# Kernel tuning notes

Measured on AMD Instinct MI355X. Metric: run time of the kernel, lower is better.

The kernel has to match this reference:

```python
import jax, jax.numpy as jnp
import numpy as np

_EPS = 1e-5
_NH, _DH = 4, 64  # heads, dim_head


def _ln(x, g, b):
    m = x.mean(-1, keepdims=True)
    v = ((x - m) ** 2).mean(-1, keepdims=True)
    return (x - m) / jnp.sqrt(v + _EPS) * g + b


def _leaky(x):
    return jnp.where(x > 0, x, 0.01 * x)


def _bn_eval(x, g, b):
    # eval-mode BatchNorm with running_mean=0, running_var=1
    return x * (g / np.sqrt(1.0 + _EPS)) + b


def setup_inputs() -> dict:
    key = jax.random.key(0)
    ks = jax.random.split(key, 20)
    B, L, S, D, T, H = 4096, 8, 877, 256, 137, 128
    f = jnp.float32

    def rn(k, shape, s=0.02):
        return jax.random.normal(k, shape, dtype=f) * s

    inp = {}
    inp['source'] = jax.random.normal(ks[0], (B, S), dtype=f)
    inp['source_neighbor'] = jax.random.normal(ks[1], (B, L, S), dtype=f)
    inp['cell_inf'] = jax.random.uniform(ks[2], (B, L + 1, 13), dtype=f)
    # encoder_rna: 877 -> 512 -> 256, Linear+BN(eval)+LeakyReLU
    inp['enc_w1'] = rn(ks[3], (S, 512)); inp['enc_b1'] = jnp.zeros((512,), f)
    inp['enc_bn1_g'] = jnp.ones((512,), f); inp['enc_bn1_b'] = jnp.zeros((512,), f)
    inp['enc_w2'] = rn(ks[4], (512, D)); inp['enc_b2'] = jnp.zeros((D,), f)
    inp['enc_bn2_g'] = jnp.ones((D,), f); inp['enc_bn2_b'] = jnp.zeros((D,), f)
    # projection_rna: Linear(256,256) + LayerNorm + ReLU
    inp['proj_w'] = rn(ks[5], (D, D)); inp['proj_b'] = jnp.zeros((D,), f)
    inp['proj_ln_g'] = jnp.ones((D,), f); inp['proj_ln_b'] = jnp.zeros((D,), f)
    # 1-layer pre-norm transformer (4 heads, dim_head 64, ff_mult 2)
    inp['attn_ln_g'] = jnp.ones((D,), f); inp['attn_ln_b'] = jnp.zeros((D,), f)
    inp['wq'] = rn(ks[6], (D, D)); inp['wk'] = rn(ks[7], (D, D)); inp['wv'] = rn(ks[8], (D, D))
    inp['wo'] = rn(ks[9], (D, D)); inp['wo_b'] = jnp.zeros((D,), f)
    inp['ff_ln_g'] = jnp.ones((D,), f); inp['ff_ln_b'] = jnp.zeros((D,), f)
    inp['ff_w1'] = rn(ks[10], (D, 2 * D)); inp['ff_b1'] = jnp.zeros((2 * D,), f)
    inp['ff_w2'] = rn(ks[11], (2 * D, D)); inp['ff_b2'] = jnp.zeros((D,), f)
    # learned tokens
    inp['token_center'] = rn(ks[12], (1, 1, D))
    inp['token_neigh_1'] = rn(ks[13], (1, 1, D))
    inp['token_neigh_2'] = rn(ks[14], (1, 1, D))
    inp['cell_tokens'] = rn(ks[15], (1, 1, 13, D))
    # 137 independent predict heads, batched: Linear(256,128)+BN+LeakyReLU+Linear(128,1,no bias)
    inp['pred_w1'] = rn(ks[16], (T, D, H)); inp['pred_b1'] = jnp.zeros((T, H), f)
    inp['pred_bn_g'] = jnp.ones((T, H), f); inp['pred_bn_b'] = jnp.zeros((T, H), f)
    inp['pred_w2'] = rn(ks[17], (T, H))
    return inp


def _forward(source, source_neighbor, cell_inf, enc_w1, enc_b1, enc_bn1_g, enc_bn1_b,
             enc_w2, enc_b2, enc_bn2_g, enc_bn2_b, proj_w, proj_b, proj_ln_g, proj_ln_b,
             attn_ln_g, attn_ln_b, wq, wk, wv, wo, wo_b, ff_ln_g, ff_ln_b,
             ff_w1, ff_b1, ff_w2, ff_b2, token_center, token_neigh_1, token_neigh_2,
             cell_tokens, pred_w1, pred_b1, pred_bn_g, pred_bn_b, pred_w2):
    B = source.shape[0]
    x = jnp.concatenate([source[:, None, :], source_neighbor], axis=1)  # [B,N,877]
    N = x.shape[1]
    l = N - 1
    half = l // 2
    valid = jnp.abs(x).sum(-1) > 0                      # [B,N] bool
    vm = valid.astype(x.dtype)[..., None]               # [B,N,1]
    D = token_center.shape[-1]
    # role tokens: center / first-half neigh / second-half neigh, masked
    role = jnp.concatenate([
        token_center,
        jnp.broadcast_to(token_neigh_1, (1, half, D)),
        jnp.broadcast_to(token_neigh_2, (1, l - half, D)),
    ], axis=1) * vm                                      # [B,N,D]
    # class tokens: weighted sum over 13 cell-type tokens, masked
    class_tok = (cell_tokens * cell_inf[..., None]).sum(-2) * vm  # [B,N,D]
    # encoder_rna (dropouts are eval identity)
    h = _leaky(_bn_eval(x @ enc_w1 + enc_b1, enc_bn1_g, enc_bn1_b))
    h = _leaky(_bn_eval(h @ enc_w2 + enc_b2, enc_bn2_g, enc_bn2_b))  # [B,N,D]
    fo = h + role + class_tok
    fo = jax.nn.relu(_ln(fo @ proj_w + proj_b, proj_ln_g, proj_ln_b))
    # local graph transformer encoder (depth=1, pre-norm, masked attention)
    hn = _ln(fo, attn_ln_g, attn_ln_b)
    q = (hn @ wq).reshape(B, N, _NH, _DH)
    k = (hn @ wk).reshape(B, N, _NH, _DH)
    v = (hn @ wv).reshape(B, N, _NH, _DH)
    scores = jnp.einsum('bihd,bjhd->bhij', q, k) * (_DH ** -0.5)
    scores = jnp.where(valid[:, None, None, :], scores, -1e9)
    attn = jax.nn.softmax(scores, axis=-1)
    o = jnp.einsum('bhij,bjhd->bihd', attn, v).reshape(B, N, _NH * _DH)
    fo = fo + o @ wo + wo_b
    hn2 = _ln(fo, ff_ln_g, ff_ln_b)
    fo = fo + jax.nn.gelu(hn2 @ ff_w1 + ff_b1) @ ff_w2 + ff_b2
    feat = fo[:, 0, :]                                   # [B,D] center token
    # 137 predict heads as one batched GEMM + fused BN/LeakyReLU
    ph = jnp.einsum('bd,tdh->bth', feat, pred_w1) + pred_b1   # [B,137,128]
    ph = _leaky(_bn_eval(ph, pred_bn_g, pred_bn_b))
    out = jnp.einsum('bth,th->bt', ph, pred_w2)               # [B,137]
    return out


def reference(source, source_neighbor, cell_inf, enc_w1, enc_b1, enc_bn1_g, enc_bn1_b,
              enc_w2, enc_b2, enc_bn2_g, enc_bn2_b, proj_w, proj_b, proj_ln_g, proj_ln_b,
              attn_ln_g, attn_ln_b, wq, wk, wv, wo, wo_b, ff_ln_g, ff_ln_b,
              ff_w1, ff_b1, ff_w2, ff_b2, token_center, token_neigh_1, token_neigh_2,
              cell_tokens, pred_w1, pred_b1, pred_bn_g, pred_bn_b, pred_w2):
    return _forward(source, source_neighbor, cell_inf, enc_w1, enc_b1, enc_bn1_g, enc_bn1_b,
                    enc_w2, enc_b2, enc_bn2_g, enc_bn2_b, proj_w, proj_b, proj_ln_g, proj_ln_b,
                    attn_ln_g, attn_ln_b, wq, wk, wv, wo, wo_b, ff_ln_g, ff_ln_b,
                    ff_w1, ff_b1, ff_w2, ff_b2, token_center, token_neigh_1, token_neigh_2,
                    cell_tokens, pred_w1, pred_b1, pred_bn_g, pred_bn_b, pred_w2)
```

## Files before the change

kernel.cpp:

```cpp
#include <hip/hip_runtime.h>
#include <hip/hip_bf16.h>
#include <math.h>

typedef __hip_bfloat16 bf16;
typedef __attribute__((ext_vector_type(8))) short short8;
typedef __attribute__((ext_vector_type(4))) float f32x4;

#define BB 4096
#define LL 8
#define NN 9
#define SS 877
#define DD 256
#define D2 512
#define TT 137
#define HH 128
#define MM (BB*NN)
#define KP1 896

__device__ __forceinline__ float lrelu(float x){ return x > 0.f ? x : 0.01f*x; }
__device__ __forceinline__ float gelu_tanh(float x){
    float x3 = x*x*x;
    float t = tanhf(0.7978845608028654f*(x + 0.044715f*x3));
    return 0.5f*x*(1.f + t);
}
__device__ __forceinline__ short f2b(float x){
    union { bf16 h; short s; } u; u.h = __float2bfloat16(x); return u.s;
}
__device__ __forceinline__ float b2f(bf16 v){ return __bfloat162float(v); }

struct SwzD { const float* src; unsigned short* dst; int K; int N; int NB; long long base; };
struct SwzTab { SwzD d[10]; long long total; };

__global__ __launch_bounds__(256) void k_swzall(SwzTab tab){
    for (long long f0 = (long long)blockIdx.x*256 + threadIdx.x; f0 < tab.total;
         f0 += (long long)gridDim.x*256){
        int di = 0;
        #pragma unroll
        for (int q = 1; q < 10; q++) if (f0 >= tab.d[q].base) di = q;
        const SwzD dd = tab.d[di];
        long long f = f0 - dd.base;
        int j = (int)(f & 7); int lane = (int)((f>>3)&63); int h = (int)((f>>9)&7);
        long long u = f>>12;
        int nb = (int)(u % dd.NB), kb = (int)(u / dd.NB);
        int k = kb*32 + ((lane>>4)<<3) + j;
        int n = nb*128 + h*16 + (lane&15);
        float v = (k < dd.K) ? dd.src[(size_t)k*dd.N + n] : 0.f;
        dd.dst[f] = (unsigned short)f2b(v);
    }
}

__global__ __launch_bounds__(256) void k_prep(const float* __restrict__ src,
                                              const float* __restrict__ srcn,
                                              float* __restrict__ vm,
                                              unsigned short* __restrict__ xbf){
    int m = blockIdx.x; int b = m / NN, n = m % NN;
    const float* row = (n == 0) ? src + (size_t)b*SS
                                : srcn + ((size_t)b*LL + (n-1))*SS;
    unsigned short* orow = xbf + (size_t)m*KP1;
    float s = 0.f;
    for (int i = threadIdx.x; i < KP1; i += 256){
        float v = (i < SS) ? row[i] : 0.f;
        s += fabsf(v);
        orow[i] = (unsigned short)f2b(v);
    }
    #pragma unroll
    for (int o = 32; o > 0; o >>= 1) s += __shfl_xor(s, o);
    __shared__ float part[4];
    if ((threadIdx.x & 63) == 0) part[threadIdx.x>>6] = s;
    __syncthreads();
    if (threadIdx.x == 0)
        vm[m] = ((part[0]+part[1]+part[2]+part[3]) > 0.f) ? 1.f : 0.f;
}

#define EPI_NONE 0
#define EPI_BN_LEAKY 1
#define EPI_RES 2
#define EPI_GELU 3

__global__ __launch_bounds__(256) void k_mgemm(
    const unsigned short* __restrict__ A, int lda,
    const unsigned short* __restrict__ Wsw, int NB, int nKb,
    const float* __restrict__ bias, const float* __restrict__ bng,
    const float* __restrict__ bnb, const float* __restrict__ res,
    int res_stride, int mode,
    float* __restrict__ out, bf16* __restrict__ outbf, int ldo)
{
    __shared__ short8 As[512];
    int row0 = blockIdx.x*128;
    int nb = blockIdx.y;
    int tid = threadIdx.x;
    int wv = tid>>6, lane = tid&63;
    int wr = wv>>1, wc = wv&1;
    int quad = lane>>4, l15 = lane&15;

    f32x4 zz = {0.f,0.f,0.f,0.f};
    f32x4 acc[4][4];
    #pragma unroll
    for (int i=0;i<4;i++){ acc[i][0]=zz; acc[i][1]=zz; acc[i][2]=zz; acc[i][3]=zz; }

    int m0 = tid>>2, k8 = tid&3;
    int m1 = m0 + 64;
    int dst0 = (m0>>4)*64 + (m0&15) + (k8<<4);
    int dst1 = (m1>>4)*64 + (m1&15) + (k8<<4);
    const short8* W8 = (const short8*)Wsw;

    for (int kb = 0; kb < nKb; kb++){
        int k0 = kb*32;
        uint4 v0 = *(const uint4*)(A + (size_t)(row0+m0)*lda + k0 + k8*8);
        uint4 v1 = *(const uint4*)(A + (size_t)(row0+m1)*lda + k0 + k8*8);
        short8 bfr[4];
        #pragma unroll
        for (int h = 0; h < 4; h++)
            bfr[h] = W8[((size_t)(kb*NB + nb)*8 + wc*4 + h)*64 + lane];
        __syncthreads();
        ((uint4*)As)[dst0] = v0;
        ((uint4*)As)[dst1] = v1;
        __syncthreads();
        #pragma unroll
        for (int i = 0; i < 4; i++){
            short8 af = As[(wr*4+i)*64 + lane];
            #pragma unroll
            for (int h = 0; h < 4; h++)
                acc[i][h] = __builtin_amdgcn_mfma_f32_16x16x32_bf16(af, bfr[h], acc[i][h], 0,0,0);
        }
    }

    const float inv = rsqrtf(1.f + 1e-5f);
    #pragma unroll
    for (int i = 0; i < 4; i++){
        int rbase = row0 + wr*64 + i*16 + quad*4;
        #pragma unroll
        for (int h = 0; h < 4; h++){
            int c = nb*128 + wc*64 + h*16 + l15;
            float bi = bias ? bias[c] : 0.f;
            #pragma unroll
            for (int reg = 0; reg < 4; reg++){
                int r = rbase + reg;
                float y = acc[i][h][reg] + bi;
                if (mode == EPI_BN_LEAKY)      y = lrelu(y*(bng[c]*inv) + bnb[c]);
                else if (mode == EPI_RES)      y += res[(size_t)r*res_stride + c];
                else if (mode == EPI_GELU)     y = gelu_tanh(y);
                if (out)   out[(size_t)r*ldo + c] = y;
                if (outbf) outbf[(size_t)r*ldo + c] = __float2bfloat16(y);
            }
        }
    }
}

__global__ __launch_bounds__(256) void k_pred_mfma(
    const unsigned short* __restrict__ feat,
    const unsigned short* __restrict__ Wsw,
    const float* __restrict__ b1, const float* __restrict__ bg,
    const float* __restrict__ bb, const float* __restrict__ w2,
    float* __restrict__ outp)
{
    __shared__ short8 As[512];
    int row0 = blockIdx.x*128;
    int t = blockIdx.y;
    int tid = threadIdx.x;
    int wv = tid>>6, lane = tid&63;
    int quad = lane>>4, l15 = lane&15;

    const float inv = rsqrtf(1.f + 1e-5f);
    float b1v[8], bgv[8], bbv[8], w2v[8];
    #pragma unroll
    for (int h = 0; h < 8; h++){
        int hc = t*HH + h*16 + l15;
        b1v[h] = b1[hc]; bgv[h] = bg[hc]*inv; bbv[h] = bb[hc]; w2v[h] = w2[hc];
    }

    f32x4 zz = {0.f,0.f,0.f,0.f};
    f32x4 acc[2][8];
    #pragma unroll
    for (int i=0;i<2;i++)
        #pragma unroll
        for (int h=0;h<8;h++) acc[i][h] = zz;

    int m0 = tid>>2, k8 = tid&3;
    int m1 = m0 + 64;
    int dst0 = (m0>>4)*64 + (m0&15) + (k8<<4);
    int dst1 = (m1>>4)*64 + (m1&15) + (k8<<4);
    const short8* W8 = (const short8*)Wsw;

    for (int kb = 0; kb < 8; kb++){
        int k0 = kb*32;
        uint4 v0 = *(const uint4*)(feat + (size_t)(row0+m0)*DD + k0 + k8*8);
        uint4 v1 = *(const uint4*)(feat + (size_t)(row0+m1)*DD + k0 + k8*8);
        short8 bfr[8];
        #pragma unroll
        for (int h = 0; h < 8; h++)
            bfr[h] = W8[((size_t)(t*8 + kb)*8 + h)*64 + lane];
        __syncthreads();
        ((uint4*)As)[dst0] = v0;
        ((uint4*)As)[dst1] = v1;
        __syncthreads();
        #pragma unroll
        for (int i = 0; i < 2; i++){
            short8 af = As[(wv*2+i)*64 + lane];
            #pragma unroll
            for (int h = 0; h < 8; h++)
                acc[i][h] = __builtin_amdgcn_mfma_f32_16x16x32_bf16(af, bfr[h], acc[i][h], 0,0,0);
        }
    }

    #pragma unroll
    for (int i = 0; i < 2; i++){
        #pragma unroll
        for (int reg = 0; reg < 4; reg++){
            float p = 0.f;
            #pragma unroll
            for (int h = 0; h < 8; h++){
                float y = (acc[i][h][reg] + b1v[h])*bgv[h] + bbv[h];
                p += lrelu(y) * w2v[h];
            }
            p += __shfl_xor(p, 1);
            p += __shfl_xor(p, 2);
            p += __shfl_xor(p, 4);
            p += __shfl_xor(p, 8);
            if (l15 == 0){
                int r = row0 + wv*32 + i*16 + quad*4 + reg;
                outp[(size_t)r*TT + t] = p;
            }
        }
    }
}

__global__ __launch_bounds__(256) void k_rolecls(const float* __restrict__ tokc,
                                                 const float* __restrict__ tokn1,
                                                 const float* __restrict__ tokn2,
                                                 const float* __restrict__ cell_tokens,
                                                 const float* __restrict__ cell_inf,
                                                 const float* __restrict__ vm,
                                                 float* __restrict__ fo,
                                                 bf16* __restrict__ fobf){
    int m = blockIdx.x, d = threadIdx.x;
    int n = m % NN;
    float v = vm[m];
    const float* role = (n == 0) ? tokc : (n <= 4 ? tokn1 : tokn2);
    float cl = 0.f;
    #pragma unroll
    for (int c = 0; c < 13; c++)
        cl += cell_inf[(size_t)m*13 + c] * cell_tokens[c*DD + d];
    float y = fo[(size_t)m*DD + d] + (role[d] + cl) * v;
    fo[(size_t)m*DD + d] = y;
    fobf[(size_t)m*DD + d] = __float2bfloat16(y);
}

__device__ __forceinline__ float blksum(float v, float* part){
    #pragma unroll
    for (int o = 32; o > 0; o >>= 1) v += __shfl_xor(v, o);
    __syncthreads();
    if ((threadIdx.x & 63) == 0) part[threadIdx.x>>6] = v;
    __syncthreads();
    return part[0]+part[1]+part[2]+part[3];
}

__global__ __launch_bounds__(256) void k_lnchain(const float* __restrict__ in,
                                                 const float* __restrict__ g1, const float* __restrict__ b1,
                                                 const float* __restrict__ g2, const float* __restrict__ b2,
                                                 float* __restrict__ fo1, bf16* __restrict__ hn){
    __shared__ float part[4];
    int m = blockIdx.x, d = threadIdx.x;
    float x = in[(size_t)m*DD + d];
    float mu = blksum(x, part) * (1.f/256.f);
    float dx = x - mu;
    float var = blksum(dx*dx, part) * (1.f/256.f);
    float y = dx * rsqrtf(var + 1e-5f) * g1[d] + b1[d];
    y = fmaxf(y, 0.f);
    fo1[(size_t)m*DD + d] = y;
    float mu2 = blksum(y, part) * (1.f/256.f);
    float dy = y - mu2;
    float var2 = blksum(dy*dy, part) * (1.f/256.f);
    hn[(size_t)m*DD + d] = __float2bfloat16(dy * rsqrtf(var2 + 1e-5f) * g2[d] + b2[d]);
}

__global__ __launch_bounds__(256) void k_ln(const float* __restrict__ in,
                                            const float* __restrict__ g, const float* __restrict__ b,
                                            bf16* __restrict__ out){
    __shared__ float part[4];
    int m = blockIdx.x, d = threadIdx.x;
    float x = in[(size_t)m*DD + d];
    float mu = blksum(x, part) * (1.f/256.f);
    float dx = x - mu;
    float var = blksum(dx*dx, part) * (1.f/256.f);
    out[(size_t)m*DD + d] = __float2bfloat16(dx * rsqrtf(var + 1e-5f) * g[d] + b[d]);
}

__global__ __launch_bounds__(256) void k_attn(const bf16* __restrict__ q,
                                              const bf16* __restrict__ k,
                                              const bf16* __restrict__ v,
                                              const float* __restrict__ vm,
                                              bf16* __restrict__ o){
    int b = blockIdx.x, t = threadIdx.x;
    __shared__ float ks[NN][DD];
    __shared__ float vs[NN][DD];
    __shared__ float qs[DD];
    __shared__ float sc[4][NN];
    __shared__ float val[NN];
    qs[t] = b2f(q[(size_t)b*DD + t]);
    for (int j = 0; j < NN; j++){
        ks[j][t] = b2f(k[((size_t)b*NN + j)*DD + t]);
        vs[j][t] = b2f(v[((size_t)b*NN + j)*DD + t]);
    }
    if (t < NN) val[t] = vm[b*NN + t];
    __syncthreads();
    if (t < 4*NN){
        int h = t / NN, j = t % NN;
        float s = 0.f;
        for (int d = 0; d < 64; d++) s += qs[h*64+d] * ks[j][h*64+d];
        s *= 0.125f;
        if (!(val[j] > 0.f)) s = -1e9f;
        sc[h][j] = s;
    }
    __syncthreads();
    if (t < 4){
        float mx = -1e30f;
        for (int j = 0; j < NN; j++) mx = fmaxf(mx, sc[t][j]);
        float den = 0.f;
        for (int j = 0; j < NN; j++){ float e = expf(sc[t][j]-mx); sc[t][j] = e; den += e; }
        float iv = 1.f/den;
        for (int j = 0; j < NN; j++) sc[t][j] *= iv;
    }
    __syncthreads();
    int h = t >> 6;
    float acc = 0.f;
    for (int j = 0; j < NN; j++) acc += sc[h][j] * vs[j][t];
    o[(size_t)b*DD + t] = __float2bfloat16(acc);
}

extern "C" void kernel_launch(void* const* d_in, const int* in_sizes, int n_in,
                              void* d_out, int out_size, void* d_ws, size_t ws_size,
                              hipStream_t stream) {
    const float* src      = (const float*)d_in[0];
    const float* srcn     = (const float*)d_in[1];
    const float* cell_inf = (const float*)d_in[2];
    const float* enc_w1   = (const float*)d_in[3];
    const float* enc_b1   = (const float*)d_in[4];
    const float* bn1g     = (const float*)d_in[5];
    const float* bn1b     = (const float*)d_in[6];
    const float* enc_w2   = (const float*)d_in[7];
    const float* enc_b2   = (const float*)d_in[8];
    const float* bn2g     = (const float*)d_in[9];
    const float* bn2b     = (const float*)d_in[10];
    const float* proj_w   = (const float*)d_in[11];
    const float* proj_b   = (const float*)d_in[12];
    const float* pln_g    = (const float*)d_in[13];
    const float* pln_b    = (const float*)d_in[14];
    const float* aln_g    = (const float*)d_in[15];
    const float* aln_b    = (const float*)d_in[16];
    const float* wq       = (const float*)d_in[17];
    const float* wk       = (const float*)d_in[18];
    const float* wv       = (const float*)d_in[19];
    const float* wo       = (const float*)d_in[20];
    const float* wo_b     = (const float*)d_in[21];
    const float* fln_g    = (const float*)d_in[22];
    const float* fln_b    = (const float*)d_in[23];
    const float* ff_w1    = (const float*)d_in[24];
    const float* ff_b1    = (const float*)d_in[25];
    const float* ff_w2    = (const float*)d_in[26];
    const float* ff_b2    = (const float*)d_in[27];
    const float* tokc     = (const float*)d_in[28];
    const float* tokn1    = (const float*)d_in[29];
    const float* tokn2    = (const float*)d_in[30];
    const float* cell_tok = (const float*)d_in[31];
    const float* pw1      = (const float*)d_in[32];
    const float* pb1      = (const float*)d_in[33];
    const float* pbg      = (const float*)d_in[34];
    const float* pbb      = (const float*)d_in[35];
    const float* pw2      = (const float*)d_in[36];
    float* out            = (float*)d_out;

    char* base = (char*)d_ws;
    size_t off = 0;
    auto alloc = [&](size_t bytes)->char*{
        char* p = base + off;
        off += (bytes + 255) & ~(size_t)255;
        return p;
    };
    bf16* sw_enc1 = (bf16*)alloc((size_t)KP1*D2*2);
    bf16* sw_enc2 = (bf16*)alloc((size_t)D2*DD*2);
    bf16* sw_proj = (bf16*)alloc((size_t)DD*DD*2);
    bf16* sw_wq   = (bf16*)alloc((size_t)DD*DD*2);
    bf16* sw_wk   = (bf16*)alloc((size_t)DD*DD*2);
    bf16* sw_wv   = (bf16*)alloc((size_t)DD*DD*2);
    bf16* sw_wo   = (bf16*)alloc((size_t)DD*DD*2);
    bf16* sw_ff1  = (bf16*)alloc((size_t)DD*D2*2);
    bf16* sw_ff2  = (bf16*)alloc((size_t)D2*DD*2);
    bf16* sw_pred = (bf16*)alloc((size_t)TT*DD*HH*2);
    float* vm    = (float*)alloc((size_t)MM*4);
    char*  xreg  = alloc((size_t)MM*KP1*2);
    bf16*  h1bf  = (bf16*)alloc((size_t)MM*D2*2);
    float* t0    = (float*)alloc((size_t)MM*DD*4);
    bf16*  hnbf  = (bf16*)alloc((size_t)MM*DD*2);
    bf16*  qbf   = (bf16*)alloc((size_t)BB*DD*2);
    bf16*  obbf  = (bf16*)alloc((size_t)BB*DD*2);
    float* fo2   = (float*)alloc((size_t)BB*DD*4);
    bf16*  hn2bf = (bf16*)alloc((size_t)BB*DD*2);
    bf16*  g1bf  = (bf16*)alloc((size_t)BB*D2*2);
    bf16*  featbf= (bf16*)alloc((size_t)BB*DD*2);
    unsigned short* xbf = (unsigned short*)xreg;
    float* fo   = (float*)xreg;
    bf16*  fobf = (bf16*)(xreg + (size_t)MM*DD*4);
    bf16* kbbf = h1bf;
    bf16* vbbf = h1bf + (size_t)MM*DD;

    dim3 blk(256);

    SwzTab tab;
    long long cum = 0;
    auto mk = [&](int slot, const float* s, bf16* d, int K, int Kpad, int N, int NB){
        tab.d[slot] = SwzD{ s, (unsigned short*)d, K, N, NB, cum };
        cum += (long long)Kpad*N;
    };
    mk(0, enc_w1, sw_enc1, SS, KP1, D2, 4);
    mk(1, enc_w2, sw_enc2, D2, D2, DD, 2);
    mk(2, proj_w, sw_proj, DD, DD, DD, 2);
    mk(3, wq,     sw_wq,   DD, DD, DD, 2);
    mk(4, wk,     sw_wk,   DD, DD, DD, 2);
    mk(5, wv,     sw_wv,   DD, DD, DD, 2);
    mk(6, wo,     sw_wo,   DD, DD, DD, 2);
    mk(7, ff_w1,  sw_ff1,  DD, DD, D2, 4);
    mk(8, ff_w2,  sw_ff2,  D2, D2, DD, 2);
    mk(9, pw1,    sw_pred, TT*DD, TT*DD, HH, 1);
    tab.total = cum;
    k_swzall<<<1024, blk, 0, stream>>>(tab);

    k_prep<<<MM, blk, 0, stream>>>(src, srcn, vm, xbf);

    k_mgemm<<<dim3(MM/128, 4), blk, 0, stream>>>(xbf, KP1,
        (const unsigned short*)sw_enc1, 4, KP1/32, enc_b1, bn1g, bn1b,
        nullptr, 0, EPI_BN_LEAKY, nullptr, h1bf, D2);
    k_mgemm<<<dim3(MM/128, 2), blk, 0, stream>>>((const unsigned short*)h1bf, D2,
        (const unsigned short*)sw_enc2, 2, 16, enc_b2, bn2g, bn2b,
        nullptr, 0, EPI_BN_LEAKY, fo, nullptr, DD);
    k_rolecls<<<MM, blk, 0, stream>>>(tokc, tokn1, tokn2, cell_tok, cell_inf, vm, fo, fobf);
    k_mgemm<<<dim3(MM/128, 2), blk, 0, stream>>>((const unsigned short*)fobf, DD,
        (const unsigned short*)sw_proj, 2, 8, proj_b, nullptr, nullptr,
        nullptr, 0, EPI_NONE, t0, nullptr, DD);
    k_lnchain<<<MM, blk, 0, stream>>>(t0, pln_g, pln_b, aln_g, aln_b, fo, hnbf);
    k_mgemm<<<dim3(MM/128, 2), blk, 0, stream>>>((const unsigned short*)hnbf, DD,
        (const unsigned short*)sw_wk, 2, 8, nullptr, nullptr, nullptr,
        nullptr, 0, EPI_NONE, nullptr, kbbf, DD);
    k_mgemm<<<dim3(MM/128, 2), blk, 0, stream>>>((const unsigned short*)hnbf, DD,
        (const unsigned short*)sw_wv, 2, 8, nullptr, nullptr, nullptr,
        nullptr, 0, EPI_NONE, nullptr, vbbf, DD);
    k_mgemm<<<dim3(BB/128, 2), blk, 0, stream>>>((const unsigned short*)hnbf, NN*DD,
        (const unsigned short*)sw_wq, 2, 8, nullptr, nullptr, nullptr,
        nullptr, 0, EPI_NONE, nullptr, qbf, DD);
    k_attn<<<BB, blk, 0, stream>>>(qbf, kbbf, vbbf, vm, obbf);
    k_mgemm<<<dim3(BB/128, 2), blk, 0, stream>>>((const unsigned short*)obbf, DD,
        (const unsigned short*)sw_wo, 2, 8, wo_b, nullptr, nullptr,
        fo, NN*DD, EPI_RES, fo2, nullptr, DD);
    k_ln<<<BB, blk, 0, stream>>>(fo2, fln_g, fln_b, hn2bf);
    k_mgemm<<<dim3(BB/128, 4), blk, 0, stream>>>((const unsigned short*)hn2bf, DD,
        (const unsigned short*)sw_ff1, 4, 8, ff_b1, nullptr, nullptr,
        nullptr, 0, EPI_GELU, nullptr, g1bf, D2);
    k_mgemm<<<dim3(BB/128, 2), blk, 0, stream>>>((const unsigned short*)g1bf, D2,
        (const unsigned short*)sw_ff2, 2, 16, ff_b2, nullptr, nullptr,
        fo2, DD, EPI_RES, nullptr, featbf, DD);
    k_pred_mfma<<<dim3(BB/128, TT), blk, 0, stream>>>((const unsigned short*)featbf,
        (const unsigned short*)sw_pred, pb1, pbg, pbb, pw2, out);
}
```

Before: 757.8 us.

## Double-buffer GEMM via direct-to-LDS loads, fuse role/cell tokens, merge K/V, batch pred heads

The generic GEMM now stages both A and swizzled weight tiles into double-buffered LDS with global_load_lds. The next k-block's load is issued while the current one is computed, which removes one barrier per iteration. The role/cell token addition is folded into the encoder-2 epilogue, which eliminates the separate k_rolecls pass over the activations. The K and V projections are merged into one GEMM with an interleaved weight layout. The predict-head kernel keeps the feature tile in registers across 8 heads per block, so A is reloaded less often. In exchange, registers and LDS use go up, and the EPI_ENC2 epilogue adds a 13-term dot product per output element.

```diff
diff --git a/kernel.cpp b/kernel.cpp
--- a/kernel.cpp
+++ b/kernel.cpp
@@ -28,7 +28,15 @@
 }
 __device__ __forceinline__ float b2f(bf16 v){ return __bfloat162float(v); }
 
-struct SwzD { const float* src; unsigned short* dst; int K; int N; int NB; long long base; };
+__device__ __forceinline__ void glds16(const void* gsrc, void* ldst){
+    __builtin_amdgcn_global_load_lds(
+        (const __attribute__((address_space(1))) void*)gsrc,
+        (__attribute__((address_space(3))) void*)ldst,
+        16, 0, 0);
+}
+
+struct SwzD { const float* src; unsigned short* dst; int K; int Nloc; int NBloc;
+              int NBt; int nbOff; long long base; };
 struct SwzTab { SwzD d[10]; long long total; };
 
 __global__ __launch_bounds__(256) void k_swzall(SwzTab tab){
@@ -41,11 +49,12 @@
         long long f = f0 - dd.base;
         int j = (int)(f & 7); int lane = (int)((f>>3)&63); int h = (int)((f>>9)&7);
         long long u = f>>12;
-        int nb = (int)(u % dd.NB), kb = (int)(u / dd.NB);
+        int nbl = (int)(u % dd.NBloc), kb = (int)(u / dd.NBloc);
         int k = kb*32 + ((lane>>4)<<3) + j;
-        int n = nb*128 + h*16 + (lane&15);
-        float v = (k < dd.K) ? dd.src[(size_t)k*dd.N + n] : 0.f;
-        dd.dst[f] = (unsigned short)f2b(v);
+        int n = nbl*128 + h*16 + (lane&15);
+        float v = (k < dd.K) ? dd.src[(size_t)k*dd.Nloc + n] : 0.f;
+        size_t dsti = ((((size_t)kb*dd.NBt + dd.nbOff + nbl)*8 + h)*64 + lane)*8 + j;
+        dd.dst[dsti] = (unsigned short)f2b(v);
     }
 }
 
@@ -76,70 +85,105 @@
 #define EPI_BN_LEAKY 1
 #define EPI_RES 2
 #define EPI_GELU 3
+#define EPI_ENC2 4
 
 __global__ __launch_bounds__(256) void k_mgemm(
     const unsigned short* __restrict__ A, int lda,
-    const unsigned short* __restrict__ Wsw, int NB, int nKb,
+    const unsigned short* __restrict__ Wsw, int NBt, int nKb,
     const float* __restrict__ bias, const float* __restrict__ bng,
     const float* __restrict__ bnb, const float* __restrict__ res,
     int res_stride, int mode,
-    float* __restrict__ out, bf16* __restrict__ outbf, int ldo)
+    float* __restrict__ out, bf16* __restrict__ outbf, int ldo,
+    const float* __restrict__ ci, const float* __restrict__ ctok,
+    const float* __restrict__ tokc, const float* __restrict__ tokn1,
+    const float* __restrict__ tokn2, const float* __restrict__ vmp)
 {
-    __shared__ short8 As[512];
+    __shared__ short8 As[2][8][64];
+    __shared__ short8 Ws[2][8][64];
+    __shared__ float ciS[128][13];
+    __shared__ float vmS[128];
     int row0 = blockIdx.x*128;
     int nb = blockIdx.y;
     int tid = threadIdx.x;
     int wv = tid>>6, lane = tid&63;
-    int wr = wv>>1, wc = wv&1;
-    int quad = lane>>4, l15 = lane&15;
+    int wr = wv>>1, wc = wv&1, quad = lane>>4, l15 = lane&15;
+
+    if (mode == EPI_ENC2){
+        for (int l = tid; l < 128*13; l += 256){
+            int r = l/13, c = l - r*13;
+            ciS[r][c] = ci[(size_t)(row0+r)*13 + c];
+        }
+        for (int l = tid; l < 128; l += 256) vmS[l] = vmp[row0+l];
+    }
 
     f32x4 zz = {0.f,0.f,0.f,0.f};
     f32x4 acc[4][4];
     #pragma unroll
     for (int i=0;i<4;i++){ acc[i][0]=zz; acc[i][1]=zz; acc[i][2]=zz; acc[i][3]=zz; }
 
-    int m0 = tid>>2, k8 = tid&3;
-    int m1 = m0 + 64;
-    int dst0 = (m0>>4)*64 + (m0&15) + (k8<<4);
-    int dst1 = (m1>>4)*64 + (m1&15) + (k8<<4);
-    const short8* W8 = (const short8*)Wsw;
-
+    #define STAGE(kb_, buf_) do{                                                   \
+        int kb__ = (kb_);                                                          \
+        for (int e = 0; e < 2; e++){                                               \
+            int grp = wv + e*4;                                                    \
+            const unsigned short* g = A + (size_t)(row0 + grp*16 + l15)*lda        \
+                                        + kb__*32 + quad*8;                        \
+            glds16(g, &As[buf_][grp][0]);                                          \
+        }                                                                          \
+        for (int e = 0; e < 2; e++){                                               \
+            int h = wv*2 + e;                                                      \
+            const unsigned short* g = Wsw +                                        \
+                ((((size_t)kb__*NBt + nb)*8 + h)*64 + lane)*8;                     \
+            glds16(g, &Ws[buf_][h][0]);                                            \
+        }                                                                          \
+    }while(0)
+
+    STAGE(0, 0);
     for (int kb = 0; kb < nKb; kb++){
-        int k0 = kb*32;
-        uint4 v0 = *(const uint4*)(A + (size_t)(row0+m0)*lda + k0 + k8*8);
-        uint4 v1 = *(const uint4*)(A + (size_t)(row0+m1)*lda + k0 + k8*8);
-        short8 bfr[4];
-        #pragma unroll
-        for (int h = 0; h < 4; h++)
-            bfr[h] = W8[((size_t)(kb*NB + nb)*8 + wc*4 + h)*64 + lane];
+        int buf = kb & 1;
         __syncthreads();
-        ((uint4*)As)[dst0] = v0;
-        ((uint4*)As)[dst1] = v1;
-        __syncthreads();
-        #pragma unroll
-        for (int i = 0; i < 4; i++){
-            short8 af = As[(wr*4+i)*64 + lane];
+        if (kb+1 < nKb) STAGE(kb+1, buf^1);
+        short8 afr[4], bfr[4];
+        #pragma unroll
+        for (int i = 0; i < 4; i++) afr[i] = As[buf][wr*4+i][lane];
+        #pragma unroll
+        for (int h = 0; h < 4; h++) bfr[h] = Ws[buf][wc*4+h][lane];
+        #pragma unroll
+        for (int i = 0; i < 4; i++)
             #pragma unroll
             for (int h = 0; h < 4; h++)
-                acc[i][h] = __builtin_amdgcn_mfma_f32_16x16x32_bf16(af, bfr[h], acc[i][h], 0,0,0);
-        }
-    }
+                acc[i][h] = __builtin_amdgcn_mfma_f32_16x16x32_bf16(afr[i], bfr[h], acc[i][h], 0,0,0);
+    }
+    #undef STAGE
 
     const float inv = rsqrtf(1.f + 1e-5f);
     #pragma unroll
     for (int i = 0; i < 4; i++){
-        int rbase = row0 + wr*64 + i*16 + quad*4;
+        int rl0 = wr*64 + i*16 + quad*4;
         #pragma unroll
         for (int h = 0; h < 4; h++){
             int c = nb*128 + wc*64 + h*16 + l15;
             float bi = bias ? bias[c] : 0.f;
             #pragma unroll
             for (int reg = 0; reg < 4; reg++){
-                int r = rbase + reg;
+                int rl = rl0 + reg;
+                int r = row0 + rl;
                 float y = acc[i][h][reg] + bi;
-                if (mode == EPI_BN_LEAKY)      y = lrelu(y*(bng[c]*inv) + bnb[c]);
-                else if (mode == EPI_RES)      y += res[(size_t)r*res_stride + c];
-                else if (mode == EPI_GELU)     y = gelu_tanh(y);
+                if (mode == EPI_BN_LEAKY){
+                    y = lrelu(y*(bng[c]*inv) + bnb[c]);
+                } else if (mode == EPI_ENC2){
+                    y = lrelu(y*(bng[c]*inv) + bnb[c]);
+                    int n = r % NN;
+                    float role = (n==0) ? tokc[c] : ((n<=4) ? tokn1[c] : tokn2[c]);
+                    float cl = 0.f;
+                    #pragma unroll
+                    for (int tck = 0; tck < 13; tck++)
+                        cl += ciS[rl][tck] * ctok[tck*DD + c];
+                    y += (role + cl) * vmS[rl];
+                } else if (mode == EPI_RES){
+                    y += res[(size_t)r*res_stride + c];
+                } else if (mode == EPI_GELU){
+                    y = gelu_tanh(y);
+                }
                 if (out)   out[(size_t)r*ldo + c] = y;
                 if (outbf) outbf[(size_t)r*ldo + c] = __float2bfloat16(y);
             }
@@ -147,103 +191,89 @@
     }
 }
 
-__global__ __launch_bounds__(256) void k_pred_mfma(
+__global__ __launch_bounds__(256) void k_pred2(
     const unsigned short* __restrict__ feat,
     const unsigned short* __restrict__ Wsw,
     const float* __restrict__ b1, const float* __restrict__ bg,
     const float* __restrict__ bb, const float* __restrict__ w2,
     float* __restrict__ outp)
 {
-    __shared__ short8 As[512];
+    __shared__ short8 Af[8][8][64];
     int row0 = blockIdx.x*128;
-    int t = blockIdx.y;
+    int t0 = blockIdx.y*8;
     int tid = threadIdx.x;
     int wv = tid>>6, lane = tid&63;
     int quad = lane>>4, l15 = lane&15;
 
+    #pragma unroll
+    for (int kb = 0; kb < 8; kb++){
+        #pragma unroll
+        for (int e = 0; e < 2; e++){
+            int grp = wv*2 + e;
+            const unsigned short* g = feat + (size_t)(row0 + grp*16 + l15)*DD
+                                           + kb*32 + quad*8;
+            glds16(g, &Af[kb][grp][0]);
+        }
+    }
+    __syncthreads();
+    short8 areg[2][8];
+    #pragma unroll
+    for (int i = 0; i < 2; i++)
+        #pragma unroll
+        for (int kb = 0; kb < 8; kb++)
+            areg[i][kb] = Af[kb][wv*2+i][lane];
+
+    const short8* W8 = (const short8*)Wsw;
     const float inv = rsqrtf(1.f + 1e-5f);
-    float b1v[8], bgv[8], bbv[8], w2v[8];
-    #pragma unroll
-    for (int h = 0; h < 8; h++){
-        int hc = t*HH + h*16 + l15;
-        b1v[h] = b1[hc]; bgv[h] = bg[hc]*inv; bbv[h] = bb[hc]; w2v[h] = w2[hc];
-    }
-
     f32x4 zz = {0.f,0.f,0.f,0.f};
-    f32x4 acc[2][8];
-    #pragma unroll
-    for (int i=0;i<2;i++)
-        #pragma unroll
-        for (int h=0;h<8;h++) acc[i][h] = zz;
-
-    int m0 = tid>>2, k8 = tid&3;
-    int m1 = m0 + 64;
-    int dst0 = (m0>>4)*64 + (m0&15) + (k8<<4);
-    int dst1 = (m1>>4)*64 + (m1&15) + (k8<<4);
-    const short8* W8 = (const short8*)Wsw;
-
-    for (int kb = 0; kb < 8; kb++){
-        int k0 = kb*32;
-        uint4 v0 = *(const uint4*)(feat + (size_t)(row0+m0)*DD + k0 + k8*8);
-        uint4 v1 = *(const uint4*)(feat + (size_t)(row0+m1)*DD + k0 + k8*8);
-        short8 bfr[8];
-        #pragma unroll
-        for (int h = 0; h < 8; h++)
-            bfr[h] = W8[((size_t)(t*8 + kb)*8 + h)*64 + lane];
-        __syncthreads();
-        ((uint4*)As)[dst0] = v0;
-        ((uint4*)As)[dst1] = v1;
-        __syncthreads();
+
+    for (int tt = 0; tt < 8; tt++){
+        int t = t0 + tt;
+        if (t >= TT) break;
+        f32x4 acc[2][8];
+        #pragma unroll
+        for (int i=0;i<2;i++)
+            #pragma unroll
+            for (int h=0;h<8;h++) acc[i][h] = zz;
+        #pragma unroll
+        for (int kb = 0; kb < 8; kb++){
+            short8 w[8];
+            #pragma unroll
+            for (int h = 0; h < 8; h++)
+                w[h] = W8[((size_t)(t*8 + kb)*8 + h)*64 + lane];
+            #pragma unroll
+            for (int i = 0; i < 2; i++)
+                #pragma unroll
+                for (int h = 0; h < 8; h++)
+                    acc[i][h] = __builtin_amdgcn_mfma_f32_16x16x32_bf16(areg[i][kb], w[h], acc[i][h], 0,0,0);
+        }
+        float b1v[8], bgv[8], bbv[8], w2v[8];
+        #pragma unroll
+        for (int h = 0; h < 8; h++){
+            int hc = t*HH + h*16 + l15;
+            b1v[h] = b1[hc]; bgv[h] = bg[hc]*inv; bbv[h] = bb[hc]; w2v[h] = w2[hc];
+        }
         #pragma unroll
         for (int i = 0; i < 2; i++){
-            short8 af = As[(wv*2+i)*64 + lane];
-            #pragma unroll
-            for (int h = 0; h < 8; h++)
-                acc[i][h] = __builtin_amdgcn_mfma_f32_16x16x32_bf16(af, bfr[h], acc[i][h], 0,0,0);
-        }
-    }
-
-    #pragma unroll
-    for (int i = 0; i < 2; i++){
-        #pragma unroll
-        for (int reg = 0; reg < 4; reg++){
-            float p = 0.f;
-            #pragma unroll
-            for (int h = 0; h < 8; h++){
-                float y = (acc[i][h][reg] + b1v[h])*bgv[h] + bbv[h];
-                p += lrelu(y) * w2v[h];
+            #pragma unroll
+            for (int reg = 0; reg < 4; reg++){
+                float p = 0.f;
+                #pragma unroll
+                for (int h = 0; h < 8; h++){
+                    float y = (acc[i][h][reg] + b1v[h])*bgv[h] + bbv[h];
+                    p += lrelu(y) * w2v[h];
+                }
+                p += __shfl_xor(p, 1);
+                p += __shfl_xor(p, 2);
+                p += __shfl_xor(p, 4);
+                p += __shfl_xor(p, 8);
+                if (l15 == 0){
+                    int r = row0 + wv*32 + i*16 + quad*4 + reg;
+                    outp[(size_t)r*TT + t] = p;
+                }
             }
-            p += __shfl_xor(p, 1);
-            p += __shfl_xor(p, 2);
-            p += __shfl_xor(p, 4);
-            p += __shfl_xor(p, 8);
-            if (l15 == 0){
-                int r = row0 + wv*32 + i*16 + quad*4 + reg;
-                outp[(size_t)r*TT + t] = p;
-            }
-        }
-    }
-}
-
-__global__ __launch_bounds__(256) void k_rolecls(const float* __restrict__ tokc,
-                                                 const float* __restrict__ tokn1,
-                                                 const float* __restrict__ tokn2,
-                                                 const float* __restrict__ cell_tokens,
-                                                 const float* __restrict__ cell_inf,
-                                                 const float* __restrict__ vm,
-                                                 float* __restrict__ fo,
-                                                 bf16* __restrict__ fobf){
-    int m = blockIdx.x, d = threadIdx.x;
-    int n = m % NN;
-    float v = vm[m];
-    const float* role = (n == 0) ? tokc : (n <= 4 ? tokn1 : tokn2);
-    float cl = 0.f;
-    #pragma unroll
-    for (int c = 0; c < 13; c++)
-        cl += cell_inf[(size_t)m*13 + c] * cell_tokens[c*DD + d];
-    float y = fo[(size_t)m*DD + d] + (role[d] + cl) * v;
-    fo[(size_t)m*DD + d] = y;
-    fobf[(size_t)m*DD + d] = __float2bfloat16(y);
+        }
+    }
 }
 
 __device__ __forceinline__ float blksum(float v, float* part){
@@ -287,8 +317,7 @@
 }
 
 __global__ __launch_bounds__(256) void k_attn(const bf16* __restrict__ q,
-                                              const bf16* __restrict__ k,
-                                              const bf16* __restrict__ v,
+                                              const bf16* __restrict__ kv,
                                               const float* __restrict__ vm,
                                               bf16* __restrict__ o){
     int b = blockIdx.x, t = threadIdx.x;
@@ -299,8 +328,8 @@
     __shared__ float val[NN];
     qs[t] = b2f(q[(size_t)b*DD + t]);
     for (int j = 0; j < NN; j++){
-        ks[j][t] = b2f(k[((size_t)b*NN + j)*DD + t]);
-        vs[j][t] = b2f(v[((size_t)b*NN + j)*DD + t]);
+        ks[j][t] = b2f(kv[((size_t)b*NN + j)*D2 + t]);
+        vs[j][t] = b2f(kv[((size_t)b*NN + j)*D2 + DD + t]);
     }
     if (t < NN) val[t] = vm[b*NN + t];
     __syncthreads();
@@ -381,8 +410,7 @@
     bf16* sw_enc2 = (bf16*)alloc((size_t)D2*DD*2);
     bf16* sw_proj = (bf16*)alloc((size_t)DD*DD*2);
     bf16* sw_wq   = (bf16*)alloc((size_t)DD*DD*2);
-    bf16* sw_wk   = (bf16*)alloc((size_t)DD*DD*2);
-    bf16* sw_wv   = (bf16*)alloc((size_t)DD*DD*2);
+    bf16* sw_kv   = (bf16*)alloc((size_t)DD*D2*2);
     bf16* sw_wo   = (bf16*)alloc((size_t)DD*DD*2);
     bf16* sw_ff1  = (bf16*)alloc((size_t)DD*D2*2);
     bf16* sw_ff2  = (bf16*)alloc((size_t)D2*DD*2);
@@ -401,27 +429,27 @@
     unsigned short* xbf = (unsigned short*)xreg;
     float* fo   = (float*)xreg;
     bf16*  fobf = (bf16*)(xreg + (size_t)MM*DD*4);
-    bf16* kbbf = h1bf;
-    bf16* vbbf = h1bf + (size_t)MM*DD;
+    bf16* kvbf  = h1bf;
 
     dim3 blk(256);
 
     SwzTab tab;
     long long cum = 0;
-    auto mk = [&](int slot, const float* s, bf16* d, int K, int Kpad, int N, int NB){
-        tab.d[slot] = SwzD{ s, (unsigned short*)d, K, N, NB, cum };
-        cum += (long long)Kpad*N;
+    auto mk = [&](int slot, const float* s, bf16* d, int K, int Kpad, int Nloc,
+                  int NBt, int nbOff){
+        tab.d[slot] = SwzD{ s, (unsigned short*)d, K, Nloc, Nloc/128, NBt, nbOff, cum };
+        cum += (long long)Kpad*Nloc;
     };
-    mk(0, enc_w1, sw_enc1, SS, KP1, D2, 4);
-    mk(1, enc_w2, sw_enc2, D2, D2, DD, 2);
-    mk(2, proj_w, sw_proj, DD, DD, DD, 2);
-    mk(3, wq,     sw_wq,   DD, DD, DD, 2);
-    mk(4, wk,     sw_wk,   DD, DD, DD, 2);
-    mk(5, wv,     sw_wv,   DD, DD, DD, 2);
-    mk(6, wo,     sw_wo,   DD, DD, DD, 2);
-    mk(7, ff_w1,  sw_ff1,  DD, DD, D2, 4);
-    mk(8, ff_w2,  sw_ff2,  D2, D2, DD, 2);
-    mk(9, pw1,    sw_pred, TT*DD, TT*DD, HH, 1);
+    mk(0, enc_w1, sw_enc1, SS, KP1, D2, 4, 0);
+    mk(1, enc_w2, sw_enc2, D2, D2, DD, 2, 0);
+    mk(2, proj_w, sw_proj, DD, DD, DD, 2, 0);
+    mk(3, wq,     sw_wq,   DD, DD, DD, 2, 0);
+    mk(4, wk,     sw_kv,   DD, DD, DD, 4, 0);
+    mk(5, wv,     sw_kv,   DD, DD, DD, 4, 2);
+    mk(6, wo,     sw_wo,   DD, DD, DD, 2, 0);
+    mk(7, ff_w1,  sw_ff1,  DD, DD, D2, 4, 0);
+    mk(8, ff_w2,  sw_ff2,  D2, D2, DD, 2, 0);
+    mk(9, pw1,    sw_pred, TT*DD, TT*DD, HH, 1, 0);
     tab.total = cum;
     k_swzall<<<1024, blk, 0, stream>>>(tab);
 
@@ -429,35 +457,39 @@
 
     k_mgemm<<<dim3(MM/128, 4), blk, 0, stream>>>(xbf, KP1,
         (const unsigned short*)sw_enc1, 4, KP1/32, enc_b1, bn1g, bn1b,
-        nullptr, 0, EPI_BN_LEAKY, nullptr, h1bf, D2);
+        nullptr, 0, EPI_BN_LEAKY, nullptr, h1bf, D2,
+        nullptr, nullptr, nullptr, nullptr, nullptr, nullptr);
     k_mgemm<<<dim3(MM/128, 2), blk, 0, stream>>>((const unsigned short*)h1bf, D2,
         (const unsigned short*)sw_enc2, 2, 16, enc_b2, bn2g, bn2b,
-        nullptr, 0, EPI_BN_LEAKY, fo, nullptr, DD);
-    k_rolecls<<<MM, blk, 0, stream>>>(tokc, tokn1, tokn2, cell_tok, cell_inf, vm, fo, fobf);
+        nullptr, 0, EPI_ENC2, fo, fobf, DD,
+        cell_inf, cell_tok, tokc, tokn1, tokn2, vm);
     k_mgemm<<<dim3(MM/128, 2), blk, 0, stream>>>((const unsigned short*)fobf, DD,
         (const unsigned short*)sw_proj, 2, 8, proj_b, nullptr, nullptr,
-        nullptr, 0, EPI_NONE, t0, nullptr, DD);
+        nullptr, 0, EPI_NONE, t0, nullptr, DD,
+        nullptr, nullptr, nullptr, nullptr, nullptr, nullptr);
     k_lnchain<<<MM, blk, 0, stream>>>(t0, pln_g, pln_b, aln_g, aln_b, fo, hnbf);
-    k_mgemm<<<dim3(MM/128, 2), blk, 0, stream>>>((const unsigned short*)hnbf, DD,
-        (const unsigned short*)sw_wk, 2, 8, nullptr, nullptr, nullptr,
-        nullptr, 0, EPI_NONE, nullptr, kbbf, DD);
-    k_mgemm<<<dim3(MM/128, 2), blk, 0, stream>>>((const unsigned short*)hnbf, DD,
-        (const unsigned short*)sw_wv, 2, 8, nullptr, nullptr, nullptr,
-        nullptr, 0, EPI_NONE, nullptr, vbbf, DD);
+    k_mgemm<<<dim3(MM/128, 4), blk, 0, stream>>>((const unsigned short*)hnbf, DD,
+        (const unsigned short*)sw_kv, 4, 8, nullptr, nullptr, nullptr,
+        nullptr, 0, EPI_NONE, nullptr, kvbf, D2,
+        nullptr, nullptr, nullptr, nullptr, nullptr, nullptr);
     k_mgemm<<<dim3(BB/128, 2), blk, 0, stream>>>((const unsigned short*)hnbf, NN*DD,
         (const unsigned short*)sw_wq, 2, 8, nullptr, nullptr, nullptr,
-        nullptr, 0, EPI_NONE, nullptr, qbf, DD);
-    k_attn<<<BB, blk, 0, stream>>>(qbf, kbbf, vbbf, vm, obbf);
+        nullptr, 0, EPI_NONE, nullptr, qbf, DD,
+        nullptr, nullptr, nullptr, nullptr, nullptr, nullptr);
+    k_attn<<<BB, blk, 0, stream>>>(qbf, kvbf, vm, obbf);
     k_mgemm<<<dim3(BB/128, 2), blk, 0, stream>>>((const unsigned short*)obbf, DD,
         (const unsigned short*)sw_wo, 2, 8, wo_b, nullptr, nullptr,
-        fo, NN*DD, EPI_RES, fo2, nullptr, DD);
+        fo, NN*DD, EPI_RES, fo2, nullptr, DD,
+        nullptr, nullptr, nullptr, nullptr, nullptr, nullptr);
     k_ln<<<BB, blk, 0, stream>>>(fo2, fln_g, fln_b, hn2bf);
     k_mgemm<<<dim3(BB/128, 4), blk, 0, stream>>>((const unsigned short*)hn2bf, DD,
         (const unsigned short*)sw_ff1, 4, 8, ff_b1, nullptr, nullptr,
-        nullptr, 0, EPI_GELU, nullptr, g1bf, D2);
+        nullptr, 0, EPI_GELU, nullptr, g1bf, D2,
+        nullptr, nullptr, nullptr, nullptr, nullptr, nullptr);
     k_mgemm<<<dim3(BB/128, 2), blk, 0, stream>>>((const unsigned short*)g1bf, D2,
         (const unsigned short*)sw_ff2, 2, 16, ff_b2, nullptr, nullptr,
-        fo2, DD, EPI_RES, nullptr, featbf, DD);
-    k_pred_mfma<<<dim3(BB/128, TT), blk, 0, stream>>>((const unsigned short*)featbf,
+        fo2, DD, EPI_RES, nullptr, featbf, DD,
+        nullptr, nullptr, nullptr, nullptr, nullptr, nullptr);
+    k_pred2<<<dim3(BB/128, (TT+7)/8), blk, 0, stream>>>((const unsigned short*)featbf,
         (const unsigned short*)sw_pred, pb1, pbg, pbb, pw2, out);
 }
```

Measured after the change: 1.010 ms. +33.3%, slower.
